# Kernel tuning notes

Measured on AMD Instinct MI355X. Metric: run time of the kernel, lower is better.

## Reference

```python
import jax, jax.numpy as jnp
import numpy as np

N, C, OUT, S, NS = 8192, 256, 256, 8, 16  # points, in_planes, out_planes, share_planes, nsample
MID = OUT  # mid_planes = out_planes // 1
H = OUT // S  # linear_w bottleneck width
EPS = 1e-5


def _bn(x, g, b, m, v):
    # inference-mode BatchNorm1d over last (channel) dim
    return (x - m) * jax.lax.rsqrt(v + EPS) * g + b


def _knn_idx(p, k):
    # squared euclidean distances, (N,N); indices of k nearest (self included)
    sq = jnp.sum(p * p, axis=1)
    d = sq[:, None] + sq[None, :] - 2.0 * (p @ p.T)
    return jax.lax.top_k(-jax.lax.stop_gradient(d), k)[1]  # (N, k) int32


def setup_inputs() -> dict:
    key = jax.random.key(0)
    ks = jax.random.split(key, 24)
    g = lambda i, shape, s=0.05: jax.random.normal(ks[i], shape, jnp.float32) * s
    u = lambda i, shape: jax.random.uniform(ks[i], shape, dtype=jnp.float32)
    return {
        'p': u(0, (N, 3)),
        'x': g(1, (N, C), 1.0),
        'w_q': g(2, (C, MID)), 'b_q': jnp.zeros((MID,), jnp.float32),
        'w_k': g(3, (C, MID)), 'b_k': jnp.zeros((MID,), jnp.float32),
        'w_v': g(4, (C, OUT)), 'b_v': jnp.zeros((OUT,), jnp.float32),
        'p_w1': g(5, (3, 3), 0.5), 'p_b1': jnp.zeros((3,), jnp.float32),
        'p_bn_g': u(6, (3,)) + 0.5, 'p_bn_b': g(7, (3,), 0.1),
        'p_bn_m': g(8, (3,), 0.1), 'p_bn_v': u(9, (3,)) + 0.5,
        'p_w2': g(10, (3, OUT), 0.5), 'p_b2': jnp.zeros((OUT,), jnp.float32),
        'w_bn1_g': u(11, (MID,)) + 0.5, 'w_bn1_b': g(12, (MID,), 0.1),
        'w_bn1_m': g(13, (MID,), 0.1), 'w_bn1_v': u(14, (MID,)) + 0.5,
        'w_l1_w': g(15, (MID, H)), 'w_l1_b': jnp.zeros((H,), jnp.float32),
        'w_bn2_g': u(16, (H,)) + 0.5, 'w_bn2_b': g(17, (H,), 0.1),
        'w_bn2_m': g(18, (H,), 0.1), 'w_bn2_v': u(19, (H,)) + 0.5,
        'w_l2_w': g(20, (H, H)), 'w_l2_b': jnp.zeros((H,), jnp.float32),
    }


def reference(p, x, w_q, b_q, w_k, b_k, w_v, b_v,
              p_w1, p_b1, p_bn_g, p_bn_b, p_bn_m, p_bn_v, p_w2, p_b2,
              w_bn1_g, w_bn1_b, w_bn1_m, w_bn1_v, w_l1_w, w_l1_b,
              w_bn2_g, w_bn2_b, w_bn2_m, w_bn2_v, w_l2_w, w_l2_b):
    # PointTransformerLayer forward (single point cloud, o = [N])
    xq = x @ w_q + b_q            # (N, MID)
    xk = x @ w_k + b_k            # (N, MID)
    xv = x @ w_v + b_v            # (N, OUT)

    idx = _knn_idx(p, NS)         # (N, NS) KNN neighbor indices
    pr_xyz = p[idx] - p[:, None, :]   # (N, NS, 3) relative coords (with_xyz=True)
    xk_g = xk[idx]                # (N, NS, MID) gathered keys
    xv_g = xv[idx]                # (N, NS, OUT) gathered values

    # linear_p: Linear(3,3) -> BN -> ReLU -> Linear(3, OUT)
    pr = jax.nn.relu(_bn(pr_xyz @ p_w1 + p_b1, p_bn_g, p_bn_b, p_bn_m, p_bn_v))
    pr = pr @ p_w2 + p_b2         # (N, NS, OUT)

    # einops reduce 'n ns (i j)->n ns j' with j=MID is identity since MID==OUT
    r_qk = xk_g - xq[:, None, :] + pr   # (N, NS, MID)

    # linear_w: BN -> ReLU -> Linear(MID,H) -> BN -> ReLU -> Linear(H,H)
    w = jax.nn.relu(_bn(r_qk, w_bn1_g, w_bn1_b, w_bn1_m, w_bn1_v)) @ w_l1_w + w_l1_b
    w = jax.nn.relu(_bn(w, w_bn2_g, w_bn2_b, w_bn2_m, w_bn2_v)) @ w_l2_w + w_l2_b
    w = jax.nn.softmax(w, axis=1)       # softmax over neighbors (dim=1)

    v = (xv_g + pr).reshape(N, NS, S, H)      # 'n ns (s i) -> n ns s i'
    out = jnp.einsum('ntsi,nti->nsi', v, w)   # weighted aggregation over neighbors
    return out.reshape(N, OUT)
```

## Files before the change

### kernel.cpp

```cpp
#include <hip/hip_runtime.h>
#include <hip/hip_bf16.h>
#include <math.h>

#define N_PTS 8192
#define C_IN  256
#define OUT_C 256
#define NSAMP 16
#define H_W   32
#define EPSBN 1e-5f
#define GDIM  8
#define NCELL (GDIM * GDIM * GDIM)
#define CAPC  768
#define CAP_H 96
#define GEMM_BLKS 384

typedef short bf16x8 __attribute__((ext_vector_type(8)));
typedef float f32x4  __attribute__((ext_vector_type(4)));

__device__ __forceinline__ float dist2(const float4 a, const float4 b) {
  float dot = a.x * b.x + a.y * b.y + a.z * b.z;
  return a.w + b.w - 2.0f * dot;
}

__device__ __forceinline__ unsigned long long make_key(float d, int j) {
  unsigned int di = __float_as_uint(d);
  unsigned int ord = ((int)di >= 0) ? (di ^ 0x80000000u) : ~di;
  return ((unsigned long long)ord << 32) | (unsigned int)j;
}

__device__ __forceinline__ void chain_insert(unsigned long long (&ak)[16], unsigned long long key) {
  if (key < ak[0]) {
    #pragma unroll
    for (int s = 0; s < 15; ++s) {
      unsigned long long mn = ak[s] < key ? ak[s] : key;
      unsigned long long nx = ak[s + 1];
      ak[s] = nx > mn ? nx : mn;
    }
    ak[15] = ak[15] < key ? ak[15] : key;
  }
}

__device__ __forceinline__ float b2f(short s) {
  return __uint_as_float(((unsigned int)(unsigned short)s) << 16);
}
__device__ __forceinline__ short f2b(float v) {
  __hip_bfloat16 h = __float2bfloat16(v);
  short s;
  __builtin_memcpy(&s, &h, 2);
  return s;
}

__global__ __launch_bounds__(256) void prep_kernel(
    const float* __restrict__ p, const float* __restrict__ x,
    const float* __restrict__ wq, const float* __restrict__ wk, const float* __restrict__ wv,
    const float* __restrict__ bq, const float* __restrict__ bk, const float* __restrict__ bv,
    const float* __restrict__ l1w, const float* __restrict__ l2w,
    const float* __restrict__ bn1g, const float* __restrict__ bn1b,
    const float* __restrict__ bn1m, const float* __restrict__ bn1v,
    float4* __restrict__ p4, __hip_bfloat16* __restrict__ Bp, float* __restrict__ biasp,
    __hip_bfloat16* __restrict__ xb,
    __hip_bfloat16* __restrict__ l1wp, __hip_bfloat16* __restrict__ l2wp,
    float* __restrict__ sc1, float* __restrict__ of1,
    int* __restrict__ cursor, int* __restrict__ pt_cell) {
  int tid = blockIdx.x * blockDim.x + threadIdx.x;
  if (tid < 262144) {
    const float* xr = &x[(size_t)tid * 8];
    float4 xa = *(const float4*)xr;
    float4 xc = *(const float4*)(xr + 4);
    bf16x8 v;
    v[0] = f2b(xa.x); v[1] = f2b(xa.y); v[2] = f2b(xa.z); v[3] = f2b(xa.w);
    v[4] = f2b(xc.x); v[5] = f2b(xc.y); v[6] = f2b(xc.z); v[7] = f2b(xc.w);
    *(bf16x8*)&xb[(size_t)tid * 8] = v;
  }
  if (tid < 48 * 32 * 16 * 8) {
    int kj = tid & 7, n = (tid >> 3) & 15, kb = (tid >> 7) & 31, nt = tid >> 12;
    int k = kb * 8 + kj, col = nt * 16 + n;
    float v;
    if (col < 256)      v = wq[k * 256 + col];
    else if (col < 512) v = wk[k * 256 + (col - 256)];
    else                v = wv[k * 256 + (col - 512)];
    Bp[tid] = __float2bfloat16(v);
  }
  if (tid < 768) {
    biasp[tid] = tid < 256 ? bq[tid] : (tid < 512 ? bk[tid - 256] : bv[tid - 512]);
  }
  if (tid < 8192) {
    int kj = tid & 7, n = (tid >> 3) & 15, kb = (tid >> 7) & 31, nt = (tid >> 12) & 1;
    int k = kb * 8 + kj, col = nt * 16 + n;
    l1wp[tid] = __float2bfloat16(l1w[k * 32 + col]);
  }
  if (tid < 1024) {
    int kj = tid & 7, n = (tid >> 3) & 15, kb = (tid >> 7) & 3, nt = (tid >> 9) & 1;
// ... 48 lines not shown
  rank[pid] = pos;
}

__global__ __launch_bounds__(256) void knn_gemm(
    const float4* __restrict__ sp4, const int* __restrict__ sidx,
    const int* __restrict__ cell_start, int* __restrict__ nbr,
    const __hip_bfloat16* __restrict__ xb, const __hip_bfloat16* __restrict__ Bp,
    const float* __restrict__ biasp, __hip_bfloat16* __restrict__ xqkv) {
  if (blockIdx.x < GEMM_BLKS) {
    const int w = threadIdx.x >> 6;
    const int lane = threadIdx.x & 63;
    const int gw = blockIdx.x * 4 + w;
    const int m0 = (gw & 127) * 64;
    const int nt4 = (gw >> 7) * 4;
    const int n = lane & 15, q = lane >> 4;

    int o[4];
    #pragma unroll
    for (int mi = 0; mi < 4; ++mi) o[mi] = sidx[m0 + mi * 16 + n];

    f32x4 acc[4][4];
    #pragma unroll
    for (int mi = 0; mi < 4; ++mi)
      #pragma unroll
      for (int ni = 0; ni < 4; ++ni) acc[mi][ni] = (f32x4){0.f, 0.f, 0.f, 0.f};

    for (int k0 = 0; k0 < 256; k0 += 32) {
      bf16x8 af[4], bfr[4];
      #pragma unroll
      for (int mi = 0; mi < 4; ++mi)
        af[mi] = *(const bf16x8*)&xb[(size_t)o[mi] * 256 + k0 + q * 8];
      #pragma unroll
      for (int ni = 0; ni < 4; ++ni)
        bfr[ni] = *(const bf16x8*)&Bp[(size_t)(nt4 + ni) * 4096 + (k0 >> 3) * 128 + q * 128 + n * 8];
      #pragma unroll
      for (int mi = 0; mi < 4; ++mi)
        #pragma unroll
        for (int ni = 0; ni < 4; ++ni)
          acc[mi][ni] = __builtin_amdgcn_mfma_f32_16x16x32_bf16(af[mi], bfr[ni], acc[mi][ni], 0, 0, 0);
    }
    #pragma unroll
    for (int ni = 0; ni < 4; ++ni) {
      int col = (nt4 + ni) * 16 + n;
      float b = biasp[col];
      #pragma unroll
      for (int mi = 0; mi < 4; ++mi)
        #pragma unroll
        for (int r = 0; r < 4; ++r)
          xqkv[(size_t)(m0 + mi * 16 + q * 4 + r) * 768 + col] = __float2bfloat16(acc[mi][ni][r] + b);
    }
    return;
  }

  const int kbid = blockIdx.x - GEMM_BLKS;
  const int cell = kbid >> 1;
  const int sub  = kbid & 1;
  const int cs = cell_start[cell], ce = cell_start[cell + 1];
  if (cs + 8 * sub >= ce) return;

  __shared__ float4 cpos[CAPC];
  __shared__ int    cidx[CAPC];
  __shared__ unsigned long long hk_s[8][CAP_H];
  __shared__ unsigned long long okey_s[8][16];
  __shared__ float tv_s[8][64];
  __shared__ int cnt_s[8];
  __shared__ int cell_s0_s[27];
  __shared__ int len_s[27];
  __shared__ int pref_s[28];
  __shared__ int nc_s, total_s;

  const int tid = threadIdx.x;
  const int hcx = cell & 7, hcy = (cell >> 3) & 7, hcz = cell >> 6;

  const int ax0 = max(hcx - 1, 0), ax1 = min(hcx + 1, GDIM - 1);
  const int ay0 = max(hcy - 1, 0), ay1 = min(hcy + 1, GDIM - 1);
  const int az0 = max(hcz - 1, 0), az1 = min(hcz + 1, GDIM - 1);
  const int nx = ax1 - ax0 + 1, ny = ay1 - ay0 + 1, nz = az1 - az0 + 1;
  const int nbc = nx * ny * nz;

  if (tid < nbc) {
    int cx = ax0 + tid % nx;
    int cy = ay0 + (tid / nx) % ny;
    int cz = az0 + tid / (nx * ny);
    int cc = (cz * GDIM + cy) * GDIM + cx;
    int s0 = cell_start[cc];
    cell_s0_s[tid] = s0;
    len_s[tid] = cell_start[cc + 1] - s0;
  }
  __syncthreads();
  if (tid == 0) {
    int off = 0;
    for (int m = 0; m < nbc; ++m) { pref_s[m] = off; off += len_s[m]; }
    pref_s[nbc] = off;
    nc_s = nbc;
    total_s = off;
  }
  __syncthreads();
  const int nc = nc_s, total = total_s;

  {
    const int grp = tid >> 5, ln = tid & 31;
    for (int m = grp; m < nbc; m += 8) {
      int base = pref_s[m], src = cell_s0_s[m];
      int lim = min(len_s[m], CAPC - base);
      for (int i = ln; i < lim; i += 32) {
        cpos[base + i] = sp4[src + i];
        cidx[base + i] = sidx[src + i];
      }
    }
  }
  __syncthreads();

  const int ptl = tid >> 5, slice = tid & 31;

  for (int p0 = cs + 8 * sub; p0 < ce; p0 += 16) {
    const int np = min(8, ce - p0);
    const bool pok = ptl < np;
    const int ld = pok ? (p0 + ptl) : cs;
    const float4 pi = sp4[ld];
    const int orig = sidx[ld];

    if (tid < 8) cnt_s[tid] = 0;
    if (tid < 128) okey_s[tid >> 4][tid & 15] = ~0ULL;
    __syncthreads();

    float t0 = 3.0e38f, t1 = 3.0e38f;
    for (int idx = slice; idx < total; idx += 32) {
      float4 q;
      if (idx < CAPC) q = cpos[idx];
      else {
        int c = 0;
        while (c + 1 < nc && pref_s[c + 1] <= idx) ++c;
        q = sp4[cell_s0_s[c] + (idx - pref_s[c])];
      }
      float d = dist2(pi, q);
      if (d < t1) {
        if (d < t0) { t1 = t0; t0 = d; } else { t1 = d; }
      }
    }
    tv_s[ptl][slice * 2]     = t0;
    tv_s[ptl][slice * 2 + 1] = t1;
    __syncthreads();

    int r0 = 0, r1 = 0;
    #pragma unroll 8
    for (int j = 0; j < 64; ++j) {
      float wv = tv_s[ptl][j];
      r0 += (wv < t0) ? 1 : 0;
      r1 += (wv < t1) ? 1 : 0;
    }
    float cand = fmaxf(r0 <= 15 ? t0 : -3.0e38f, r1 <= 15 ? t1 : -3.0e38f);
    cand = fmaxf(cand, __shfl_xor(cand, 1, 64));
    cand = fmaxf(cand, __shfl_xor(cand, 2, 64));
    cand = fmaxf(cand, __shfl_xor(cand, 4, 64));
    cand = fmaxf(cand, __shfl_xor(cand, 8, 64));
    cand = fmaxf(cand, __shfl_xor(cand, 16, 64));
    const float d16 = cand;

    const float rg = sqrtf(fmaxf(d16, 0.f)) * 1.001f + 1e-4f;
    const int lx = (int)fminf(fmaxf(floorf((pi.x - rg) * GDIM), 0.f), (float)(GDIM - 1));
    const int ux = (int)fminf(fmaxf(floorf((pi.x + rg) * GDIM), 0.f), (float)(GDIM - 1));
    const int ly = (int)fminf(fmaxf(floorf((pi.y - rg) * GDIM), 0.f), (float)(GDIM - 1));
    const int uy = (int)fminf(fmaxf(floorf((pi.y + rg) * GDIM), 0.f), (float)(GDIM - 1));
    const int lz = (int)fminf(fmaxf(floorf((pi.z - rg) * GDIM), 0.f), (float)(GDIM - 1));
    const int uz = (int)fminf(fmaxf(floorf((pi.z + rg) * GDIM), 0.f), (float)(GDIM - 1));
    const bool trigger = (lx < ax0 || ux > ax1 || ly < ay0 || uy > ay1 || lz < az0 || uz > az1);

    if (pok) {
      for (int idx = slice; idx < total; idx += 32) {
        float4 q;
        int qi;
        if (idx < CAPC) { q = cpos[idx]; qi = cidx[idx]; }
        else {
          int c = 0;
          while (c + 1 < nc && pref_s[c + 1] <= idx) ++c;
          int g = cell_s0_s[c] + (idx - pref_s[c]);
          q = sp4[g]; qi = sidx[g];
        }
        float d = dist2(pi, q);
        if (d <= d16) {
          int pos = atomicAdd(&cnt_s[ptl], 1);
          if (pos < CAP_H) hk_s[ptl][pos] = make_key(d, qi);
        }
      }
      if (trigger) {
        for (int cz = lz; cz <= uz; ++cz)
          for (int cy = ly; cy <= uy; ++cy)
            for (int cx = lx; cx <= ux; ++cx) {
              if (cx >= ax0 && cx <= ax1 && cy >= ay0 && cy <= ay1 && cz >= az0 && cz <= az1)
                continue;
              int cc = (cz * GDIM + cy) * GDIM + cx;
              int s0 = cell_start[cc], e0 = cell_start[cc + 1];
              for (int k = s0 + slice; k < e0; k += 32) {
                float d = dist2(pi, sp4[k]);
                if (d <= d16) {
                  int pos = atomicAdd(&cnt_s[ptl], 1);
                  if (pos < CAP_H) hk_s[ptl][pos] = make_key(d, sidx[k]);
                }
              }
            }
      }
    }
    __syncthreads();

    const int cntr = cnt_s[ptl];
    const bool overflow = cntr > CAP_H;
    const int cnt = overflow ? 0 : cntr;

    if (pok) {
      for (int i = slice; i < cnt; i += 32) {
        unsigned long long key = hk_s[ptl][i];
        int rk = 0;
        for (int j = 0; j < cnt; ++j) rk += (hk_s[ptl][j] < key) ? 1 : 0;
        if (rk < 16) okey_s[ptl][rk] = key;
      }
    }
    __syncthreads();

    if (!overflow) {
      if (pok && slice < 16) {
        unsigned long long key = okey_s[ptl][15 - slice];
        nbr[orig * NSAMP + slice] = (int)(key & 0xFFFFFFFFu);
      }
    } else if (pok && slice == 0) {
      unsigned long long akm[16];
      #pragma unroll
      for (int s = 0; s < 16; ++s) akm[s] = ~0ULL;
      for (int idx2 = 0; idx2 < total; ++idx2) {
        float4 q; int qi;
        if (idx2 < CAPC) { q = cpos[idx2]; qi = cidx[idx2]; }
        else {
          int c = 0;
          while (c + 1 < nc && pref_s[c + 1] <= idx2) ++c;
          int g = cell_s0_s[c] + (idx2 - pref_s[c]);
          q = sp4[g]; qi = sidx[g];
        }
        chain_insert(akm, make_key(dist2(pi, q), qi));
      }
      float r;
      if (akm[0] == ~0ULL) r = 1e9f;
      else {
        unsigned int ord = (unsigned int)(akm[0] >> 32);
        unsigned int di = (ord & 0x80000000u) ? (ord ^ 0x80000000u) : ~ord;
        float dd = __uint_as_float(di);
        r = sqrtf(fmaxf(dd, 0.f)) * 1.001f + 1e-4f;
      }
      int flx = (int)fminf(fmaxf(floorf((pi.x - r) * GDIM), 0.f), (float)(GDIM - 1));
      int fux = (int)fminf(fmaxf(floorf((pi.x + r) * GDIM), 0.f), (float)(GDIM - 1));
      int fly = (int)fminf(fmaxf(floorf((pi.y - r) * GDIM), 0.f), (float)(GDIM - 1));
      int fuy = (int)fminf(fmaxf(floorf((pi.y + r) * GDIM), 0.f), (float)(GDIM - 1));
      int flz = (int)fminf(fmaxf(floorf((pi.z - r) * GDIM), 0.f), (float)(GDIM - 1));
      int fuz = (int)fminf(fmaxf(floorf((pi.z + r) * GDIM), 0.f), (float)(GDIM - 1));
      for (int cz = flz; cz <= fuz; ++cz)
        for (int cy = fly; cy <= fuy; ++cy)
          for (int cx = flx; cx <= fux; ++cx) {
            if (cx >= ax0 && cx <= ax1 && cy >= ay0 && cy <= ay1 && cz >= az0 && cz <= az1)
              continue;
            int cc = (cz * GDIM + cy) * GDIM + cx;
            int s0 = cell_start[cc], e0 = cell_start[cc + 1];
            for (int k = s0; k < e0; ++k) {
              float4 q = sp4[k];
              chain_insert(akm, make_key(dist2(pi, q), sidx[k]));
            }
          }
      #pragma unroll
      for (int s = 0; s < 16; ++s) nbr[orig * NSAMP + s] = (int)(akm[s] & 0xFFFFFFFFu);
    }
    __syncthreads();
  }
}

__global__ __launch_bounds__(256) void fused_pt(
    const float4* __restrict__ sp4, const int* __restrict__ sidx, const int* __restrict__ rank,
    const __hip_bfloat16* __restrict__ xqkv, const int* __restrict__ nbr,
    const float* __restrict__ pw1, const float* __restrict__ pb1,
    const float* __restrict__ pbng, const float* __restrict__ pbnb,
    const float* __restrict__ pbnm, const float* __restrict__ pbnv,
    const float* __restrict__ pw2, const float* __restrict__ pb2,
    const float* __restrict__ sc1, const float* __restrict__ of1,
    const __hip_bfloat16* __restrict__ l1wp, const float* __restrict__ l1b,
    const float* __restrict__ bn2g, const float* __restrict__ bn2b,
    const float* __restrict__ bn2m, const float* __restrict__ bn2v,
    const __hip_bfloat16* __restrict__ l2wp, const float* __restrict__ l2b,
    float* __restrict__ out) {
  __shared__ __align__(16) __hip_bfloat16 a_s[2][NSAMP][264];
  __shared__ __align__(16) __hip_bfloat16 h1_s[2][NSAMP][40];
  __shared__ float w_s[2][NSAMP][33];
  __shared__ float q3_s[2][NSAMP][4];
  __shared__ int jn[2][NSAMP];
  __shared__ float psum[2][2][264];
  __shared__ int iorig[2];

  const int b0 = blockIdx.x * 2;
  const int tid = threadIdx.x;

  if (tid < 32) {
    int spt = tid >> 4, t = tid & 15;
    int b = b0 + spt;
    int i = sidx[b];
    if (t == 0) iorig[spt] = i;
    int j = nbr[i * NSAMP + t];
    int k = rank[j];
    jn[spt][t] = k;
    float4 pj = sp4[k];
    float4 pc = sp4[b];
    float rx = pj.x - pc.x;
    float ry = pj.y - pc.y;
    float rz = pj.z - pc.z;
    #pragma unroll
    for (int c3 = 0; c3 < 3; ++c3) {
      float t2 = rx * pw1[0 * 3 + c3] + ry * pw1[1 * 3 + c3] + rz * pw1[2 * 3 + c3] + pb1[c3];
      t2 = (t2 - pbnm[c3]) * rsqrtf(pbnv[c3] + EPSBN) * pbng[c3] + pbnb[c3];
      q3_s[spt][t][c3] = fmaxf(t2, 0.f);
    }
  }
  __syncthreads();

  const int pt = tid >> 7;
  const int t127 = tid & 127;
  const int g = t127 >> 5;
  const int cg = (t127 & 31) * 8;
  const int b = b0 + pt;

  float xqv[8], s1v[8], o1v[8], w20v[8], w21v[8], w22v[8], pb2v[8];
  {
    bf16x8 xq8 = *(const bf16x8*)&xqkv[(size_t)b * 768 + cg];
    #pragma unroll
    for (int u = 0; u < 8; ++u) {
      int c = cg + u;
      xqv[u] = b2f(xq8[u]);
      s1v[u] = sc1[c];
      o1v[u] = of1[c];
      w20v[u] = pw2[c];
      w21v[u] = pw2[256 + c];
      w22v[u] = pw2[512 + c];
      pb2v[u] = pb2[c];
    }
  }

  #pragma unroll
  for (int pass = 0; pass < 4; ++pass) {
    int t = g + pass * 4;
    int k = jn[pt][t];
    float q30 = q3_s[pt][t][0], q31 = q3_s[pt][t][1], q32 = q3_s[pt][t][2];
    bf16x8 xk8 = *(const bf16x8*)&xqkv[(size_t)k * 768 + 256 + cg];
    bf16x8 av;
    #pragma unroll
    for (int u = 0; u < 8; ++u) {
      float prv = q30 * w20v[u] + q31 * w21v[u] + q32 * w22v[u] + pb2v[u];
      float r = b2f(xk8[u]) - xqv[u] + prv;
      av[u] = f2b(fmaxf(r * s1v[u] + o1v[u], 0.f));
    }
    *(bf16x8*)&a_s[pt][t][cg] = av;
  }
  __syncthreads();

  const int w = tid >> 6;
  const int lane = tid & 63;
  const int mpt = w >> 1, hh = w & 1;
  const int nn = lane & 15, q = lane >> 4;
  {
    f32x4 acc = {0.f, 0.f, 0.f, 0.f};
    #pragma unroll
    for (int k0 = 0; k0 < 256; k0 += 32) {
      bf16x8 a = *(const bf16x8*)&a_s[mpt][nn][k0 + q * 8];
      bf16x8 bb = *(const bf16x8*)&l1wp[hh * 4096 + (k0 >> 3) * 128 + q * 128 + nn * 8];
      acc = __builtin_amdgcn_mfma_f32_16x16x32_bf16(a, bb, acc, 0, 0, 0);
    }
    int h = hh * 16 + nn;
    float s2 = bn2g[h] * rsqrtf(bn2v[h] + EPSBN);
    float o2 = bn2b[h] - bn2m[h] * s2;
    float l1bh = l1b[h];
    #pragma unroll
    for (int r = 0; r < 4; ++r)
      h1_s[mpt][q * 4 + r][h] = __float2bfloat16(fmaxf((acc[r] + l1bh) * s2 + o2, 0.f));
  }
  __syncthreads();

  {
    bf16x8 a = *(const bf16x8*)&h1_s[mpt][nn][q * 8];
    bf16x8 bb = *(const bf16x8*)&l2wp[hh * 512 + q * 128 + nn * 8];
    f32x4 z = {0.f, 0.f, 0.f, 0.f};
    f32x4 d = __builtin_amdgcn_mfma_f32_16x16x32_bf16(a, bb, z, 0, 0, 0);
    int h = hh * 16 + nn;
    float l2bh = l2b[h];
    #pragma unroll
    for (int r = 0; r < 4; ++r) w_s[mpt][q * 4 + r][h] = d[r] + l2bh;
  }
  __syncthreads();

  if (tid < 64) {
    int spt = tid >> 5, h = tid & 31;
    float m = -1e30f;
    #pragma unroll
    for (int t = 0; t < NSAMP; ++t) m = fmaxf(m, w_s[spt][t][h]);
    float e[NSAMP];
    float ssum = 0.f;
    #pragma unroll
    for (int t = 0; t < NSAMP; ++t) { e[t] = __expf(w_s[spt][t][h] - m); ssum += e[t]; }
    float inv = 1.f / ssum;
    #pragma unroll
    for (int t = 0; t < NSAMP; ++t) w_s[spt][t][h] = e[t] * inv;
  }
  __syncthreads();

  const int hb = cg & 31;
  float acc8[8];
  #pragma unroll
  for (int u = 0; u < 8; ++u) acc8[u] = 0.f;
  #pragma unroll
  for (int pass = 0; pass < 4; ++pass) {
    int t = g + pass * 4;
    int k = jn[pt][t];
    float q30 = q3_s[pt][t][0], q31 = q3_s[pt][t][1], q32 = q3_s[pt][t][2];
    bf16x8 xv8 = *(const bf16x8*)&xqkv[(size_t)k * 768 + 512 + cg];
    #pragma unroll
    for (int u = 0; u < 8; ++u) {
      float prv = q30 * w20v[u] + q31 * w21v[u] + q32 * w22v[u] + pb2v[u];
      acc8[u] += (b2f(xv8[u]) + prv) * w_s[pt][t][hb + u];
    }
  }
  #pragma unroll
  for (int u = 0; u < 8; ++u) acc8[u] += __shfl_xor(acc8[u], 32, 64);
  if ((lane >> 5) == 0) {
    #pragma unroll
    for (int u = 0; u < 8; ++u) psum[mpt][hh][cg + u] = acc8[u];
  }
  __syncthreads();
  {
    int opt = tid >> 7;
    int c0 = (tid & 127) * 2;
    float v0 = psum[opt][0][c0] + psum[opt][1][c0];
    float v1 = psum[opt][0][c0 + 1] + psum[opt][1][c0 + 1];
    int io = iorig[opt];
    *(float2*)&out[(size_t)io * OUT_C + c0] = make_float2(v0, v1);
  }
}

extern "C" void kernel_launch(void* const* d_in, const int* in_sizes, int n_in,
                              void* d_out, int out_size, void* d_ws, size_t ws_size,
                              hipStream_t stream) {
  const float* p    = (const float*)d_in[0];
  const float* x    = (const float*)d_in[1];
  const float* wq   = (const float*)d_in[2];
  const float* bq   = (const float*)d_in[3];
  const float* wk   = (const float*)d_in[4];
  const float* bk   = (const float*)d_in[5];
  const float* wv   = (const float*)d_in[6];
  const float* bv   = (const float*)d_in[7];
  const float* pw1  = (const float*)d_in[8];
  const float* pb1  = (const float*)d_in[9];
  const float* pbng = (const float*)d_in[10];
  const float* pbnb = (const float*)d_in[11];
  const float* pbnm = (const float*)d_in[12];
  const float* pbnv = (const float*)d_in[13];
  const float* pw2  = (const float*)d_in[14];
  const float* pb2  = (const float*)d_in[15];
  const float* bn1g = (const float*)d_in[16];
  const float* bn1b = (const float*)d_in[17];
  const float* bn1m = (const float*)d_in[18];
  const float* bn1v = (const float*)d_in[19];
  const float* l1w  = (const float*)d_in[20];
  const float* l1b  = (const float*)d_in[21];
  const float* bn2g = (const float*)d_in[22];
  const float* bn2b = (const float*)d_in[23];
  const float* bn2m = (const float*)d_in[24];
  const float* bn2v = (const float*)d_in[25];
  const float* l2w  = (const float*)d_in[26];
  const float* l2b  = (const float*)d_in[27];
  float* out = (float*)d_out;

  char* ws = (char*)d_ws;
  float4* p4       = (float4*)(ws + 0x000000);
  float*  biasp    = (float*)(ws + 0x040000);
  int*    cursor   = (int*)(ws + 0x042800);
  int*    cell_st  = (int*)(ws + 0x043000);
  int*    pt_cell  = (int*)(ws + 0x044000);
  float4* sp4      = (float4*)(ws + 0x050000);
  int*    sidx     = (int*)(ws + 0x070000);
  __hip_bfloat16* l1wp = (__hip_bfloat16*)(ws + 0x080000);
  __hip_bfloat16* l2wp = (__hip_bfloat16*)(ws + 0x084000);
  float*  sc1      = (float*)(ws + 0x085000);
  float*  of1      = (float*)(ws + 0x085800);
  int*    rank     = (int*)(ws + 0x088000);
  int*    nbr      = (int*)(ws + 0x090000);
  __hip_bfloat16* Bp   = (__hip_bfloat16*)(ws + 0x110000);
  __hip_bfloat16* xb   = (__hip_bfloat16*)(ws + 0x170000);
  __hip_bfloat16* xqkv = (__hip_bfloat16*)(ws + 0x570000);

  prep_kernel<<<dim3(1024), dim3(256), 0, stream>>>(
      p, x, wq, wk, wv, bq, bk, bv, l1w, l2w, bn1g, bn1b, bn1m, bn1v,
      p4, Bp, biasp, xb, l1wp, l2wp, sc1, of1, cursor, pt_cell);
  scatter_scan<<<dim3(16), dim3(512), 0, stream>>>(
      p4, pt_cell, cell_st, cursor, sp4, sidx, rank);
  knn_gemm<<<dim3(GEMM_BLKS + NCELL * 2), dim3(256), 0, stream>>>(
      sp4, sidx, cell_st, nbr, xb, Bp, biasp, xqkv);
  fused_pt<<<dim3(N_PTS / 2), dim3(256), 0, stream>>>(
      sp4, sidx, rank, xqkv, nbr, pw1, pb1, pbng, pbnb, pbnm, pbnv, pw2, pb2,
      sc1, of1, l1wp, l1b, bn2g, bn2b, bn2m, bn2v, l2wp, l2b, out);
}
```

Before: 197.9 us.

## Assign one wavefront per query point in KNN and drop shared-memory cell staging

The KNN part of the combined kernel is restructured so that each 64-lane wavefront handles one query point, with 2048 blocks of 4 points instead of two blocks per grid cell. Points are read directly from global memory over contiguous x-runs of the neighbouring cells, and the block-wide staging into shared memory and the __syncthreads barriers are removed. Candidate collection uses ballot/popcount compaction in place of shared atomics, and the final top-16 ranking is done with cross-lane shuffles. This removes per-cell load imbalance and barrier cost, but trades shared-memory reuse for repeated global/L2 reads and lowers the overflow buffer cap to 64.

```diff
diff --git a/kernel.cpp b/kernel.cpp
--- a/kernel.cpp
+++ b/kernel.cpp
@@ -10,9 +10,9 @@
 #define EPSBN 1e-5f
 #define GDIM  8
 #define NCELL (GDIM * GDIM * GDIM)
-#define CAPC  768
-#define CAP_H 96
+#define CAP_W 64
 #define GEMM_BLKS 384
+#define KNN_BLKS (N_PTS / 4)
 
 typedef short bf16x8 __attribute__((ext_vector_type(8)));
 typedef float f32x4  __attribute__((ext_vector_type(4)));
@@ -38,6 +38,18 @@
     }
     ak[15] = ak[15] < key ? ak[15] : key;
   }
+}
+
+__device__ __forceinline__ void ins2(float d, float& t0, float& t1) {
+  if (d < t1) {
+    if (d < t0) { t1 = t0; t0 = d; } else { t1 = d; }
+  }
+}
+
+__device__ __forceinline__ unsigned long long shfl64(unsigned long long v, int src) {
+  int lo = __shfl((int)(unsigned int)(v & 0xFFFFFFFFu), src, 64);
+  int hi = __shfl((int)(unsigned int)(v >> 32), src, 64);
+  return ((unsigned long long)(unsigned int)hi << 32) | (unsigned int)lo;
 }
 
 __device__ __forceinline__ float b2f(short s) {
@@ -192,221 +204,157 @@
     return;
   }
 
-  const int kbid = blockIdx.x - GEMM_BLKS;
-  const int cell = kbid >> 1;
-  const int sub  = kbid & 1;
-  const int cs = cell_start[cell], ce = cell_start[cell + 1];
-  if (cs + 8 * sub >= ce) return;
-
-  __shared__ float4 cpos[CAPC];
-  __shared__ int    cidx[CAPC];
-  __shared__ unsigned long long hk_s[8][CAP_H];
-  __shared__ unsigned long long okey_s[8][16];
-  __shared__ float tv_s[8][64];
-  __shared__ int cnt_s[8];
-  __shared__ int cell_s0_s[27];
-  __shared__ int len_s[27];
-  __shared__ int pref_s[28];
-  __shared__ int nc_s, total_s;
-
-  const int tid = threadIdx.x;
-  const int hcx = cell & 7, hcy = (cell >> 3) & 7, hcz = cell >> 6;
-
+  __shared__ unsigned long long buf_s[4][CAP_W];
+
+  const int wv = threadIdx.x >> 6;
+  const int lane = threadIdx.x & 63;
+  const int pid = (blockIdx.x - GEMM_BLKS) * 4 + wv;
+
+  const float4 pi = sp4[pid];
+  const int orig = sidx[pid];
+
+  const int hcx = min(GDIM - 1, max(0, (int)(pi.x * GDIM)));
+  const int hcy = min(GDIM - 1, max(0, (int)(pi.y * GDIM)));
+  const int hcz = min(GDIM - 1, max(0, (int)(pi.z * GDIM)));
   const int ax0 = max(hcx - 1, 0), ax1 = min(hcx + 1, GDIM - 1);
   const int ay0 = max(hcy - 1, 0), ay1 = min(hcy + 1, GDIM - 1);
   const int az0 = max(hcz - 1, 0), az1 = min(hcz + 1, GDIM - 1);
-  const int nx = ax1 - ax0 + 1, ny = ay1 - ay0 + 1, nz = az1 - az0 + 1;
-  const int nbc = nx * ny * nz;
-
-  if (tid < nbc) {
-    int cx = ax0 + tid % nx;
-    int cy = ay0 + (tid / nx) % ny;
-    int cz = az0 + tid / (nx * ny);
-    int cc = (cz * GDIM + cy) * GDIM + cx;
-    int s0 = cell_start[cc];
-    cell_s0_s[tid] = s0;
-    len_s[tid] = cell_start[cc + 1] - s0;
-  }
-  __syncthreads();
-  if (tid == 0) {
-    int off = 0;
-    for (int m = 0; m < nbc; ++m) { pref_s[m] = off; off += len_s[m]; }
-    pref_s[nbc] = off;
-    nc_s = nbc;
-    total_s = off;
-  }
-  __syncthreads();
-  const int nc = nc_s, total = total_s;
-
-  {
-    const int grp = tid >> 5, ln = tid & 31;
-    for (int m = grp; m < nbc; m += 8) {
-      int base = pref_s[m], src = cell_s0_s[m];
-      int lim = min(len_s[m], CAPC - base);
-      for (int i = ln; i < lim; i += 32) {
-        cpos[base + i] = sp4[src + i];
-        cidx[base + i] = sidx[src + i];
+
+  float t0 = 3.0e38f, t1 = 3.0e38f;
+  for (int cz = az0; cz <= az1; ++cz)
+    for (int cy = ay0; cy <= ay1; ++cy) {
+      int base = (cz * GDIM + cy) * GDIM;
+      int s = cell_start[base + ax0];
+      int e = cell_start[base + ax1 + 1];
+      for (int k = s + lane; k < e; k += 64) {
+        float d = dist2(pi, sp4[k]);
+        ins2(d, t0, t1);
       }
     }
-  }
-  __syncthreads();
-
-  const int ptl = tid >> 5, slice = tid & 31;
-
-  for (int p0 = cs + 8 * sub; p0 < ce; p0 += 16) {
-    const int np = min(8, ce - p0);
-    const bool pok = ptl < np;
-    const int ld = pok ? (p0 + ptl) : cs;
-    const float4 pi = sp4[ld];
-    const int orig = sidx[ld];
-
-    if (tid < 8) cnt_s[tid] = 0;
-    if (tid < 128) okey_s[tid >> 4][tid & 15] = ~0ULL;
-    __syncthreads();
-
-    float t0 = 3.0e38f, t1 = 3.0e38f;
-    for (int idx = slice; idx < total; idx += 32) {
-      float4 q;
-      if (idx < CAPC) q = cpos[idx];
-      else {
-        int c = 0;
-        while (c + 1 < nc && pref_s[c + 1] <= idx) ++c;
-        q = sp4[cell_s0_s[c] + (idx - pref_s[c])];
+
+  int r0 = 0, r1 = (t0 < t1) ? 1 : 0;
+  #pragma unroll 7
+  for (int s = 1; s < 64; ++s) {
+    float o0 = __shfl(t0, (lane + s) & 63, 64);
+    float o1 = __shfl(t1, (lane + s) & 63, 64);
+    r0 += (o0 < t0) ? 1 : 0;
+    r0 += (o1 < t0) ? 1 : 0;
+    r1 += (o0 < t1) ? 1 : 0;
+    r1 += (o1 < t1) ? 1 : 0;
+  }
+  float cand = fmaxf(r0 <= 15 ? t0 : -3.0e38f, r1 <= 15 ? t1 : -3.0e38f);
+  cand = fmaxf(cand, __shfl_xor(cand, 1, 64));
+  cand = fmaxf(cand, __shfl_xor(cand, 2, 64));
+  cand = fmaxf(cand, __shfl_xor(cand, 4, 64));
+  cand = fmaxf(cand, __shfl_xor(cand, 8, 64));
+  cand = fmaxf(cand, __shfl_xor(cand, 16, 64));
+  cand = fmaxf(cand, __shfl_xor(cand, 32, 64));
+  const float d16 = cand;
+
+  const float rg = sqrtf(fmaxf(d16, 0.f)) * 1.001f + 1e-4f;
+  const int lx = (int)fminf(fmaxf(floorf((pi.x - rg) * GDIM), 0.f), (float)(GDIM - 1));
+  const int ux = (int)fminf(fmaxf(floorf((pi.x + rg) * GDIM), 0.f), (float)(GDIM - 1));
+  const int ly = (int)fminf(fmaxf(floorf((pi.y - rg) * GDIM), 0.f), (float)(GDIM - 1));
+  const int uy = (int)fminf(fmaxf(floorf((pi.y + rg) * GDIM), 0.f), (float)(GDIM - 1));
+  const int lz = (int)fminf(fmaxf(floorf((pi.z - rg) * GDIM), 0.f), (float)(GDIM - 1));
+  const int uz = (int)fminf(fmaxf(floorf((pi.z + rg) * GDIM), 0.f), (float)(GDIM - 1));
+  const bool trigger = (lx < ax0 || ux > ax1 || ly < ay0 || uy > ay1 || lz < az0 || uz > az1);
+
+  const unsigned long long lmask = (1ULL << lane) - 1ULL;
+  int cnt = 0;
+  for (int cz = az0; cz <= az1; ++cz)
+    for (int cy = ay0; cy <= ay1; ++cy) {
+      int base = (cz * GDIM + cy) * GDIM;
+      int s = cell_start[base + ax0];
+      int e = cell_start[base + ax1 + 1];
+      int trips = (e - s + 63) >> 6;
+      for (int t = 0; t < trips; ++t) {
+        int idx = s + t * 64 + lane;
+        bool valid = idx < e;
+        int safei = valid ? idx : s;
+        float d = dist2(pi, sp4[safei]);
+        bool pred = valid && (d <= d16);
+        unsigned long long m = __ballot(pred);
+        if (pred) {
+          int pos = cnt + __popcll(m & lmask);
+          if (pos < CAP_W) buf_s[wv][pos] = make_key(d, sidx[idx]);
+        }
+        cnt += __popcll(m);
       }
-      float d = dist2(pi, q);
-      if (d < t1) {
-        if (d < t0) { t1 = t0; t0 = d; } else { t1 = d; }
+    }
+  if (trigger) {
+    for (int cz = lz; cz <= uz; ++cz)
+      for (int cy = ly; cy <= uy; ++cy)
+        for (int cx = lx; cx <= ux; ++cx) {
+          if (cx >= ax0 && cx <= ax1 && cy >= ay0 && cy <= ay1 && cz >= az0 && cz <= az1)
+            continue;
+          int cc = (cz * GDIM + cy) * GDIM + cx;
+          int s = cell_start[cc], e = cell_start[cc + 1];
+          int trips = (e - s + 63) >> 6;
+          for (int t = 0; t < trips; ++t) {
+            int idx = s + t * 64 + lane;
+            bool valid = idx < e;
+            int safei = valid ? idx : s;
+            float d = dist2(pi, sp4[safei]);
+            bool pred = valid && (d <= d16);
+            unsigned long long m = __ballot(pred);
+            if (pred) {
+              int pos = cnt + __popcll(m & lmask);
+              if (pos < CAP_W) buf_s[wv][pos] = make_key(d, sidx[idx]);
+            }
+            cnt += __popcll(m);
+          }
+        }
+  }
+
+  if (cnt <= CAP_W) {
+    unsigned long long key = (lane < cnt) ? buf_s[wv][lane] : ~0ULL;
+    int rk = 0;
+    #pragma unroll 7
+    for (int s = 1; s < 64; ++s) {
+      unsigned long long ko = shfl64(key, (lane + s) & 63);
+      rk += (ko < key) ? 1 : 0;
+    }
+    if (lane < cnt && rk < 16)
+      nbr[orig * NSAMP + (15 - rk)] = (int)(key & 0xFFFFFFFFu);
+  } else if (lane == 0) {
+    unsigned long long akm[16];
+    #pragma unroll
+    for (int s = 0; s < 16; ++s) akm[s] = ~0ULL;
+    for (int cz = az0; cz <= az1; ++cz)
+      for (int cy = ay0; cy <= ay1; ++cy) {
+        int base = (cz * GDIM + cy) * GDIM;
+        int s = cell_start[base + ax0];
+        int e = cell_start[base + ax1 + 1];
+        for (int k = s; k < e; ++k)
+          chain_insert(akm, make_key(dist2(pi, sp4[k]), sidx[k]));
       }
-    }
-    tv_s[ptl][slice * 2]     = t0;
-    tv_s[ptl][slice * 2 + 1] = t1;
-    __syncthreads();
-
-    int r0 = 0, r1 = 0;
-    #pragma unroll 8
-    for (int j = 0; j < 64; ++j) {
-      float wv = tv_s[ptl][j];
-      r0 += (wv < t0) ? 1 : 0;
-      r1 += (wv < t1) ? 1 : 0;
-    }
-    float cand = fmaxf(r0 <= 15 ? t0 : -3.0e38f, r1 <= 15 ? t1 : -3.0e38f);
-    cand = fmaxf(cand, __shfl_xor(cand, 1, 64));
-    cand = fmaxf(cand, __shfl_xor(cand, 2, 64));
-    cand = fmaxf(cand, __shfl_xor(cand, 4, 64));
-    cand = fmaxf(cand, __shfl_xor(cand, 8, 64));
-    cand = fmaxf(cand, __shfl_xor(cand, 16, 64));
-    const float d16 = cand;
-
-    const float rg = sqrtf(fmaxf(d16, 0.f)) * 1.001f + 1e-4f;
-    const int lx = (int)fminf(fmaxf(floorf((pi.x - rg) * GDIM), 0.f), (float)(GDIM - 1));
-    const int ux = (int)fminf(fmaxf(floorf((pi.x + rg) * GDIM), 0.f), (float)(GDIM - 1));
-    const int ly = (int)fminf(fmaxf(floorf((pi.y - rg) * GDIM), 0.f), (float)(GDIM - 1));
-    const int uy = (int)fminf(fmaxf(floorf((pi.y + rg) * GDIM), 0.f), (float)(GDIM - 1));
-    const int lz = (int)fminf(fmaxf(floorf((pi.z - rg) * GDIM), 0.f), (float)(GDIM - 1));
-    const int uz = (int)fminf(fmaxf(floorf((pi.z + rg) * GDIM), 0.f), (float)(GDIM - 1));
-    const bool trigger = (lx < ax0 || ux > ax1 || ly < ay0 || uy > ay1 || lz < az0 || uz > az1);
-
-    if (pok) {
-      for (int idx = slice; idx < total; idx += 32) {
-        float4 q;
-        int qi;
-        if (idx < CAPC) { q = cpos[idx]; qi = cidx[idx]; }
-        else {
-          int c = 0;
-          while (c + 1 < nc && pref_s[c + 1] <= idx) ++c;
-          int g = cell_s0_s[c] + (idx - pref_s[c]);
-          q = sp4[g]; qi = sidx[g];
+    float r;
+    if (akm[0] == ~0ULL) r = 1e9f;
+    else {
+      unsigned int ord = (unsigned int)(akm[0] >> 32);
+      unsigned int di = (ord & 0x80000000u) ? (ord ^ 0x80000000u) : ~ord;
+      float dd = __uint_as_float(di);
+      r = sqrtf(fmaxf(dd, 0.f)) * 1.001f + 1e-4f;
+    }
+    int flx = (int)fminf(fmaxf(floorf((pi.x - r) * GDIM), 0.f), (float)(GDIM - 1));
+    int fux = (int)fminf(fmaxf(floorf((pi.x + r) * GDIM), 0.f), (float)(GDIM - 1));
+    int fly = (int)fminf(fmaxf(floorf((pi.y - r) * GDIM), 0.f), (float)(GDIM - 1));
+    int fuy = (int)fminf(fmaxf(floorf((pi.y + r) * GDIM), 0.f), (float)(GDIM - 1));
+    int flz = (int)fminf(fmaxf(floorf((pi.z - r) * GDIM), 0.f), (float)(GDIM - 1));
+    int fuz = (int)fminf(fmaxf(floorf((pi.z + r) * GDIM), 0.f), (float)(GDIM - 1));
+    for (int cz = flz; cz <= fuz; ++cz)
+      for (int cy = fly; cy <= fuy; ++cy)
+        for (int cx = flx; cx <= fux; ++cx) {
+          if (cx >= ax0 && cx <= ax1 && cy >= ay0 && cy <= ay1 && cz >= az0 && cz <= az1)
+            continue;
+          int cc = (cz * GDIM + cy) * GDIM + cx;
+          int s0 = cell_start[cc], e0 = cell_start[cc + 1];
+          for (int k = s0; k < e0; ++k)
+            chain_insert(akm, make_key(dist2(pi, sp4[k]), sidx[k]));
         }
-        float d = dist2(pi, q);
-        if (d <= d16) {
-          int pos = atomicAdd(&cnt_s[ptl], 1);
-          if (pos < CAP_H) hk_s[ptl][pos] = make_key(d, qi);
-        }
-      }
-      if (trigger) {
-        for (int cz = lz; cz <= uz; ++cz)
-          for (int cy = ly; cy <= uy; ++cy)
-            for (int cx = lx; cx <= ux; ++cx) {
-              if (cx >= ax0 && cx <= ax1 && cy >= ay0 && cy <= ay1 && cz >= az0 && cz <= az1)
-                continue;
-              int cc = (cz * GDIM + cy) * GDIM + cx;
-              int s0 = cell_start[cc], e0 = cell_start[cc + 1];
-              for (int k = s0 + slice; k < e0; k += 32) {
-                float d = dist2(pi, sp4[k]);
-                if (d <= d16) {
-                  int pos = atomicAdd(&cnt_s[ptl], 1);
-                  if (pos < CAP_H) hk_s[ptl][pos] = make_key(d, sidx[k]);
-                }
-              }
-            }
-      }
-    }
-    __syncthreads();
-
-    const int cntr = cnt_s[ptl];
-    const bool overflow = cntr > CAP_H;
-    const int cnt = overflow ? 0 : cntr;
-
-    if (pok) {
-      for (int i = slice; i < cnt; i += 32) {
-        unsigned long long key = hk_s[ptl][i];
-        int rk = 0;
-        for (int j = 0; j < cnt; ++j) rk += (hk_s[ptl][j] < key) ? 1 : 0;
-        if (rk < 16) okey_s[ptl][rk] = key;
-      }
-    }
-    __syncthreads();
-
-    if (!overflow) {
-      if (pok && slice < 16) {
-        unsigned long long key = okey_s[ptl][15 - slice];
-        nbr[orig * NSAMP + slice] = (int)(key & 0xFFFFFFFFu);
-      }
-    } else if (pok && slice == 0) {
-      unsigned long long akm[16];
-      #pragma unroll
-      for (int s = 0; s < 16; ++s) akm[s] = ~0ULL;
-      for (int idx2 = 0; idx2 < total; ++idx2) {
-        float4 q; int qi;
-        if (idx2 < CAPC) { q = cpos[idx2]; qi = cidx[idx2]; }
-        else {
-          int c = 0;
-          while (c + 1 < nc && pref_s[c + 1] <= idx2) ++c;
-          int g = cell_s0_s[c] + (idx2 - pref_s[c]);
-          q = sp4[g]; qi = sidx[g];
-        }
-        chain_insert(akm, make_key(dist2(pi, q), qi));
-      }
-      float r;
-      if (akm[0] == ~0ULL) r = 1e9f;
-      else {
-        unsigned int ord = (unsigned int)(akm[0] >> 32);
-        unsigned int di = (ord & 0x80000000u) ? (ord ^ 0x80000000u) : ~ord;
-        float dd = __uint_as_float(di);
-        r = sqrtf(fmaxf(dd, 0.f)) * 1.001f + 1e-4f;
-      }
-      int flx = (int)fminf(fmaxf(floorf((pi.x - r) * GDIM), 0.f), (float)(GDIM - 1));
-      int fux = (int)fminf(fmaxf(floorf((pi.x + r) * GDIM), 0.f), (float)(GDIM - 1));
-      int fly = (int)fminf(fmaxf(floorf((pi.y - r) * GDIM), 0.f), (float)(GDIM - 1));
-      int fuy = (int)fminf(fmaxf(floorf((pi.y + r) * GDIM), 0.f), (float)(GDIM - 1));
-      int flz = (int)fminf(fmaxf(floorf((pi.z - r) * GDIM), 0.f), (float)(GDIM - 1));
-      int fuz = (int)fminf(fmaxf(floorf((pi.z + r) * GDIM), 0.f), (float)(GDIM - 1));
-      for (int cz = flz; cz <= fuz; ++cz)
-        for (int cy = fly; cy <= fuy; ++cy)
-          for (int cx = flx; cx <= fux; ++cx) {
-            if (cx >= ax0 && cx <= ax1 && cy >= ay0 && cy <= ay1 && cz >= az0 && cz <= az1)
-              continue;
-            int cc = (cz * GDIM + cy) * GDIM + cx;
-            int s0 = cell_start[cc], e0 = cell_start[cc + 1];
-            for (int k = s0; k < e0; ++k) {
-              float4 q = sp4[k];
-              chain_insert(akm, make_key(dist2(pi, q), sidx[k]));
-            }
-          }
-      #pragma unroll
-      for (int s = 0; s < 16; ++s) nbr[orig * NSAMP + s] = (int)(akm[s] & 0xFFFFFFFFu);
-    }
-    __syncthreads();
+    #pragma unroll
+    for (int s = 0; s < 16; ++s) nbr[orig * NSAMP + s] = (int)(akm[s] & 0xFFFFFFFFu);
   }
 }
 
@@ -633,7 +581,7 @@
       p4, Bp, biasp, xb, l1wp, l2wp, sc1, of1, cursor, pt_cell);
   scatter_scan<<<dim3(16), dim3(512), 0, stream>>>(
       p4, pt_cell, cell_st, cursor, sp4, sidx, rank);
-  knn_gemm<<<dim3(GEMM_BLKS + NCELL * 2), dim3(256), 0, stream>>>(
+  knn_gemm<<<dim3(GEMM_BLKS + KNN_BLKS), dim3(256), 0, stream>>>(
       sp4, sidx, cell_st, nbr, xb, Bp, biasp, xqkv);
   fused_pt<<<dim3(N_PTS / 2), dim3(256), 0, stream>>>(
       sp4, sidx, rank, xqkv, nbr, pw1, pb1, pbng, pbnb, pbnm, pbnv, pw2, pb2,
```

Measured after the change: 210.3 us. 6.3% more time.

## Make fused_pt wave-per-point, replacing block barriers with wave-local LDS waits

Applied to the files above, without the earlier changes.

The fused attention kernel now assigns one 64-lane wave to each point (four points per block) instead of two points per block split across waves. Because each wave owns its own shared-memory slices, the __syncthreads barriers become wave-local lgkmcnt waits, and the cross-wave partial-sum reduction through LDS is removed. Each wave now does both H halves of the MFMA GEMMs and all 16 neighbors of the final aggregation, so per-thread work and register use go up. The KNN inner loop change is cosmetic.

```diff
diff --git a/kernel.cpp b/kernel.cpp
--- a/kernel.cpp
+++ b/kernel.cpp
@@ -15,7 +15,14 @@
 #define GEMM_BLKS 384
 
 typedef short bf16x8 __attribute__((ext_vector_type(8)));
+typedef short bf16x4 __attribute__((ext_vector_type(4)));
 typedef float f32x4  __attribute__((ext_vector_type(4)));
+
+#define WSYNC() do { \
+  __builtin_amdgcn_sched_barrier(0); \
+  asm volatile("s_waitcnt lgkmcnt(0)" ::: "memory"); \
+  __builtin_amdgcn_sched_barrier(0); \
+} while (0)
 
 __device__ __forceinline__ float dist2(const float4 a, const float4 b) {
   float dot = a.x * b.x + a.y * b.y + a.z * b.z;
@@ -398,10 +405,8 @@
               continue;
             int cc = (cz * GDIM + cy) * GDIM + cx;
             int s0 = cell_start[cc], e0 = cell_start[cc + 1];
-            for (int k = s0; k < e0; ++k) {
-              float4 q = sp4[k];
-              chain_insert(akm, make_key(dist2(pi, q), sidx[k]));
-            }
+            for (int k = s0; k < e0; ++k)
+              chain_insert(akm, make_key(dist2(pi, sp4[k]), sidx[k]));
           }
       #pragma unroll
       for (int s = 0; s < 16; ++s) nbr[orig * NSAMP + s] = (int)(akm[s] & 0xFFFFFFFFu);
@@ -423,25 +428,22 @@
     const float* __restrict__ bn2m, const float* __restrict__ bn2v,
     const __hip_bfloat16* __restrict__ l2wp, const float* __restrict__ l2b,
     float* __restrict__ out) {
-  __shared__ __align__(16) __hip_bfloat16 a_s[2][NSAMP][264];
-  __shared__ __align__(16) __hip_bfloat16 h1_s[2][NSAMP][40];
-  __shared__ float w_s[2][NSAMP][33];
-  __shared__ float q3_s[2][NSAMP][4];
-  __shared__ int jn[2][NSAMP];
-  __shared__ float psum[2][2][264];
-  __shared__ int iorig[2];
-
-  const int b0 = blockIdx.x * 2;
-  const int tid = threadIdx.x;
-
-  if (tid < 32) {
-    int spt = tid >> 4, t = tid & 15;
-    int b = b0 + spt;
-    int i = sidx[b];
-    if (t == 0) iorig[spt] = i;
-    int j = nbr[i * NSAMP + t];
+  __shared__ __align__(16) __hip_bfloat16 a_s[4][NSAMP][264];
+  __shared__ __align__(16) __hip_bfloat16 h1_s[4][NSAMP][40];
+  __shared__ float w_s[4][NSAMP][33];
+  __shared__ float q3_s[4][NSAMP][4];
+  __shared__ int jn_s[4][NSAMP];
+
+  const int wv = threadIdx.x >> 6;
+  const int lane = threadIdx.x & 63;
+  const int b = blockIdx.x * 4 + wv;
+  const int io = sidx[b];
+
+  if (lane < 16) {
+    int t = lane;
+    int j = nbr[io * NSAMP + t];
     int k = rank[j];
-    jn[spt][t] = k;
+    jn_s[wv][t] = k;
     float4 pj = sp4[k];
     float4 pc = sp4[b];
     float rx = pj.x - pc.x;
@@ -451,129 +453,161 @@
     for (int c3 = 0; c3 < 3; ++c3) {
       float t2 = rx * pw1[0 * 3 + c3] + ry * pw1[1 * 3 + c3] + rz * pw1[2 * 3 + c3] + pb1[c3];
       t2 = (t2 - pbnm[c3]) * rsqrtf(pbnv[c3] + EPSBN) * pbng[c3] + pbnb[c3];
-      q3_s[spt][t][c3] = fmaxf(t2, 0.f);
-    }
-  }
-  __syncthreads();
-
-  const int pt = tid >> 7;
-  const int t127 = tid & 127;
-  const int g = t127 >> 5;
-  const int cg = (t127 & 31) * 8;
-  const int b = b0 + pt;
-
-  float xqv[8], s1v[8], o1v[8], w20v[8], w21v[8], w22v[8], pb2v[8];
+      q3_s[wv][t][c3] = fmaxf(t2, 0.f);
+    }
+  }
+  WSYNC();
+
   {
-    bf16x8 xq8 = *(const bf16x8*)&xqkv[(size_t)b * 768 + cg];
-    #pragma unroll
-    for (int u = 0; u < 8; ++u) {
-      int c = cg + u;
-      xqv[u] = b2f(xq8[u]);
-      s1v[u] = sc1[c];
-      o1v[u] = of1[c];
-      w20v[u] = pw2[c];
-      w21v[u] = pw2[256 + c];
-      w22v[u] = pw2[512 + c];
-      pb2v[u] = pb2[c];
-    }
-  }
-
-  #pragma unroll
-  for (int pass = 0; pass < 4; ++pass) {
-    int t = g + pass * 4;
-    int k = jn[pt][t];
-    float q30 = q3_s[pt][t][0], q31 = q3_s[pt][t][1], q32 = q3_s[pt][t][2];
-    bf16x8 xk8 = *(const bf16x8*)&xqkv[(size_t)k * 768 + 256 + cg];
-    bf16x8 av;
-    #pragma unroll
-    for (int u = 0; u < 8; ++u) {
-      float prv = q30 * w20v[u] + q31 * w21v[u] + q32 * w22v[u] + pb2v[u];
-      float r = b2f(xk8[u]) - xqv[u] + prv;
-      av[u] = f2b(fmaxf(r * s1v[u] + o1v[u], 0.f));
-    }
-    *(bf16x8*)&a_s[pt][t][cg] = av;
-  }
-  __syncthreads();
-
-  const int w = tid >> 6;
-  const int lane = tid & 63;
-  const int mpt = w >> 1, hh = w & 1;
+    const int c0 = (lane & 15) * 16;
+    bf16x8 xq0 = *(const bf16x8*)&xqkv[(size_t)b * 768 + c0];
+    bf16x8 xq1 = *(const bf16x8*)&xqkv[(size_t)b * 768 + c0 + 8];
+    float xqv[16], s1v[16], o1v[16], w20v[16], w21v[16], w22v[16], pb2v[16];
+    #pragma unroll
+    for (int u = 0; u < 8; ++u) { xqv[u] = b2f(xq0[u]); xqv[8 + u] = b2f(xq1[u]); }
+    #pragma unroll
+    for (int u4 = 0; u4 < 4; ++u4) {
+      float4 a0 = *(const float4*)&sc1[c0 + u4 * 4];
+      float4 a1 = *(const float4*)&of1[c0 + u4 * 4];
+      float4 a2 = *(const float4*)&pw2[c0 + u4 * 4];
+      float4 a3 = *(const float4*)&pw2[256 + c0 + u4 * 4];
+      float4 a4 = *(const float4*)&pw2[512 + c0 + u4 * 4];
+      float4 a5 = *(const float4*)&pb2[c0 + u4 * 4];
+      s1v[u4*4+0]=a0.x; s1v[u4*4+1]=a0.y; s1v[u4*4+2]=a0.z; s1v[u4*4+3]=a0.w;
+      o1v[u4*4+0]=a1.x; o1v[u4*4+1]=a1.y; o1v[u4*4+2]=a1.z; o1v[u4*4+3]=a1.w;
+      w20v[u4*4+0]=a2.x; w20v[u4*4+1]=a2.y; w20v[u4*4+2]=a2.z; w20v[u4*4+3]=a2.w;
+      w21v[u4*4+0]=a3.x; w21v[u4*4+1]=a3.y; w21v[u4*4+2]=a3.z; w21v[u4*4+3]=a3.w;
+      w22v[u4*4+0]=a4.x; w22v[u4*4+1]=a4.y; w22v[u4*4+2]=a4.z; w22v[u4*4+3]=a4.w;
+      pb2v[u4*4+0]=a5.x; pb2v[u4*4+1]=a5.y; pb2v[u4*4+2]=a5.z; pb2v[u4*4+3]=a5.w;
+    }
+    #pragma unroll
+    for (int pass = 0; pass < 4; ++pass) {
+      int t = (lane >> 4) + pass * 4;
+      int k = jn_s[wv][t];
+      float q30 = q3_s[wv][t][0], q31 = q3_s[wv][t][1], q32 = q3_s[wv][t][2];
+      bf16x8 xk0 = *(const bf16x8*)&xqkv[(size_t)k * 768 + 256 + c0];
+      bf16x8 xk1 = *(const bf16x8*)&xqkv[(size_t)k * 768 + 256 + c0 + 8];
+      bf16x8 av0, av1;
+      #pragma unroll
+      for (int u = 0; u < 8; ++u) {
+        float prv = q30 * w20v[u] + q31 * w21v[u] + q32 * w22v[u] + pb2v[u];
+        float r = b2f(xk0[u]) - xqv[u] + prv;
+        av0[u] = f2b(fmaxf(r * s1v[u] + o1v[u], 0.f));
+      }
+      #pragma unroll
+      for (int u = 0; u < 8; ++u) {
+        float prv = q30 * w20v[8+u] + q31 * w21v[8+u] + q32 * w22v[8+u] + pb2v[8+u];
+        float r = b2f(xk1[u]) - xqv[8+u] + prv;
+        av1[u] = f2b(fmaxf(r * s1v[8+u] + o1v[8+u], 0.f));
+      }
+      *(bf16x8*)&a_s[wv][t][c0] = av0;
+      *(bf16x8*)&a_s[wv][t][c0 + 8] = av1;
+    }
+  }
+  WSYNC();
+
   const int nn = lane & 15, q = lane >> 4;
+
   {
-    f32x4 acc = {0.f, 0.f, 0.f, 0.f};
+    f32x4 acc0 = {0.f, 0.f, 0.f, 0.f};
+    f32x4 acc1 = {0.f, 0.f, 0.f, 0.f};
     #pragma unroll
     for (int k0 = 0; k0 < 256; k0 += 32) {
-      bf16x8 a = *(const bf16x8*)&a_s[mpt][nn][k0 + q * 8];
-      bf16x8 bb = *(const bf16x8*)&l1wp[hh * 4096 + (k0 >> 3) * 128 + q * 128 + nn * 8];
-      acc = __builtin_amdgcn_mfma_f32_16x16x32_bf16(a, bb, acc, 0, 0, 0);
-    }
-    int h = hh * 16 + nn;
-    float s2 = bn2g[h] * rsqrtf(bn2v[h] + EPSBN);
-    float o2 = bn2b[h] - bn2m[h] * s2;
-    float l1bh = l1b[h];
-    #pragma unroll
-    for (int r = 0; r < 4; ++r)
-      h1_s[mpt][q * 4 + r][h] = __float2bfloat16(fmaxf((acc[r] + l1bh) * s2 + o2, 0.f));
-  }
-  __syncthreads();
+      bf16x8 a = *(const bf16x8*)&a_s[wv][nn][k0 + q * 8];
+      bf16x8 b0 = *(const bf16x8*)&l1wp[(k0 >> 3) * 128 + q * 128 + nn * 8];
+      bf16x8 b1 = *(const bf16x8*)&l1wp[4096 + (k0 >> 3) * 128 + q * 128 + nn * 8];
+      acc0 = __builtin_amdgcn_mfma_f32_16x16x32_bf16(a, b0, acc0, 0, 0, 0);
+      acc1 = __builtin_amdgcn_mfma_f32_16x16x32_bf16(a, b1, acc1, 0, 0, 0);
+    }
+    {
+      int h = nn;
+      float s2 = bn2g[h] * rsqrtf(bn2v[h] + EPSBN);
+      float o2 = bn2b[h] - bn2m[h] * s2;
+      float l1bh = l1b[h];
+      #pragma unroll
+      for (int r = 0; r < 4; ++r)
+        h1_s[wv][q * 4 + r][h] = __float2bfloat16(fmaxf((acc0[r] + l1bh) * s2 + o2, 0.f));
+    }
+    {
+      int h = 16 + nn;
+      float s2 = bn2g[h] * rsqrtf(bn2v[h] + EPSBN);
+      float o2 = bn2b[h] - bn2m[h] * s2;
+      float l1bh = l1b[h];
+      #pragma unroll
+      for (int r = 0; r < 4; ++r)
+        h1_s[wv][q * 4 + r][h] = __float2bfloat16(fmaxf((acc1[r] + l1bh) * s2 + o2, 0.f));
+    }
+  }
+  WSYNC();
 
   {
-    bf16x8 a = *(const bf16x8*)&h1_s[mpt][nn][q * 8];
-    bf16x8 bb = *(const bf16x8*)&l2wp[hh * 512 + q * 128 + nn * 8];
+    bf16x8 a2 = *(const bf16x8*)&h1_s[wv][nn][q * 8];
+    bf16x8 bb0 = *(const bf16x8*)&l2wp[q * 128 + nn * 8];
+    bf16x8 bb1 = *(const bf16x8*)&l2wp[512 + q * 128 + nn * 8];
     f32x4 z = {0.f, 0.f, 0.f, 0.f};
-    f32x4 d = __builtin_amdgcn_mfma_f32_16x16x32_bf16(a, bb, z, 0, 0, 0);
-    int h = hh * 16 + nn;
-    float l2bh = l2b[h];
-    #pragma unroll
-    for (int r = 0; r < 4; ++r) w_s[mpt][q * 4 + r][h] = d[r] + l2bh;
-  }
-  __syncthreads();
-
-  if (tid < 64) {
-    int spt = tid >> 5, h = tid & 31;
+    f32x4 d0 = __builtin_amdgcn_mfma_f32_16x16x32_bf16(a2, bb0, z, 0, 0, 0);
+    f32x4 d1 = __builtin_amdgcn_mfma_f32_16x16x32_bf16(a2, bb1, z, 0, 0, 0);
+    float l2b0 = l2b[nn], l2b1 = l2b[16 + nn];
+    #pragma unroll
+    for (int r = 0; r < 4; ++r) {
+      w_s[wv][q * 4 + r][nn] = d0[r] + l2b0;
+      w_s[wv][q * 4 + r][16 + nn] = d1[r] + l2b1;
+    }
+  }
+  WSYNC();
+
+  if (lane < 32) {
+    int h = lane;
     float m = -1e30f;
     #pragma unroll
-    for (int t = 0; t < NSAMP; ++t) m = fmaxf(m, w_s[spt][t][h]);
+    for (int t = 0; t < NSAMP; ++t) m = fmaxf(m, w_s[wv][t][h]);
     float e[NSAMP];
     float ssum = 0.f;
     #pragma unroll
-    for (int t = 0; t < NSAMP; ++t) { e[t] = __expf(w_s[spt][t][h] - m); ssum += e[t]; }
+    for (int t = 0; t < NSAMP; ++t) { e[t] = __expf(w_s[wv][t][h] - m); ssum += e[t]; }
     float inv = 1.f / ssum;
     #pragma unroll
-    for (int t = 0; t < NSAMP; ++t) w_s[spt][t][h] = e[t] * inv;
-  }
-  __syncthreads();
-
-  const int hb = cg & 31;
-  float acc8[8];
-  #pragma unroll
-  for (int u = 0; u < 8; ++u) acc8[u] = 0.f;
-  #pragma unroll
-  for (int pass = 0; pass < 4; ++pass) {
-    int t = g + pass * 4;
-    int k = jn[pt][t];
-    float q30 = q3_s[pt][t][0], q31 = q3_s[pt][t][1], q32 = q3_s[pt][t][2];
-    bf16x8 xv8 = *(const bf16x8*)&xqkv[(size_t)k * 768 + 512 + cg];
-    #pragma unroll
-    for (int u = 0; u < 8; ++u) {
-      float prv = q30 * w20v[u] + q31 * w21v[u] + q32 * w22v[u] + pb2v[u];
-      acc8[u] += (b2f(xv8[u]) + prv) * w_s[pt][t][hb + u];
-    }
-  }
-  #pragma unroll
-  for (int u = 0; u < 8; ++u) acc8[u] += __shfl_xor(acc8[u], 32, 64);
-  if ((lane >> 5) == 0) {
-    #pragma unroll
-    for (int u = 0; u < 8; ++u) psum[mpt][hh][cg + u] = acc8[u];
-  }
-  __syncthreads();
+    for (int t = 0; t < NSAMP; ++t) w_s[wv][t][h] = e[t] * inv;
+  }
+  WSYNC();
+
   {
-    int opt = tid >> 7;
-    int c0 = (tid & 127) * 2;
-    float v0 = psum[opt][0][c0] + psum[opt][1][c0];
-    float v1 = psum[opt][0][c0 + 1] + psum[opt][1][c0 + 1];
-    int io = iorig[opt];
-    *(float2*)&out[(size_t)io * OUT_C + c0] = make_float2(v0, v1);
+    const int pc0 = lane * 4;
+    const int hb = pc0 & 31;
+    float4 t20 = *(const float4*)&pw2[pc0];
+    float4 t21 = *(const float4*)&pw2[256 + pc0];
+    float4 t22 = *(const float4*)&pw2[512 + pc0];
+    float4 tb2 = *(const float4*)&pb2[pc0];
+    float w20p[4] = {t20.x, t20.y, t20.z, t20.w};
+    float w21p[4] = {t21.x, t21.y, t21.z, t21.w};
+    float w22p[4] = {t22.x, t22.y, t22.z, t22.w};
+    float pb2p[4] = {tb2.x, tb2.y, tb2.z, tb2.w};
+    float S[4][4];
+    #pragma unroll
+    for (int g = 0; g < 4; ++g)
+      #pragma unroll
+      for (int cc = 0; cc < 4; ++cc) S[g][cc] = 0.f;
+    #pragma unroll
+    for (int pass = 0; pass < 4; ++pass) {
+      #pragma unroll
+      for (int g = 0; g < 4; ++g) {
+        int t = g + pass * 4;
+        int k = jn_s[wv][t];
+        float q30 = q3_s[wv][t][0], q31 = q3_s[wv][t][1], q32 = q3_s[wv][t][2];
+        bf16x4 xv4 = *(const bf16x4*)&xqkv[(size_t)k * 768 + 512 + pc0];
+        #pragma unroll
+        for (int cc = 0; cc < 4; ++cc) {
+          float prv = q30 * w20p[cc] + q31 * w21p[cc] + q32 * w22p[cc] + pb2p[cc];
+          S[g][cc] += (b2f(xv4[cc]) + prv) * w_s[wv][t][hb + cc];
+        }
+      }
+    }
+    float4 res;
+    res.x = (S[0][0] + S[1][0]) + (S[2][0] + S[3][0]);
+    res.y = (S[0][1] + S[1][1]) + (S[2][1] + S[3][1]);
+    res.z = (S[0][2] + S[1][2]) + (S[2][2] + S[3][2]);
+    res.w = (S[0][3] + S[1][3]) + (S[2][3] + S[3][3]);
+    *(float4*)&out[(size_t)io * OUT_C + pc0] = res;
   }
 }
 
@@ -635,7 +669,7 @@
       p4, pt_cell, cell_st, cursor, sp4, sidx, rank);
   knn_gemm<<<dim3(GEMM_BLKS + NCELL * 2), dim3(256), 0, stream>>>(
       sp4, sidx, cell_st, nbr, xb, Bp, biasp, xqkv);
-  fused_pt<<<dim3(N_PTS / 2), dim3(256), 0, stream>>>(
+  fused_pt<<<dim3(N_PTS / 4), dim3(256), 0, stream>>>(
       sp4, sidx, rank, xqkv, nbr, pw1, pb1, pbng, pbnb, pbnm, pbnv, pw2, pb2,
       sc1, of1, l1wp, l1b, bn2g, bn2b, bn2m, bn2v, l2wp, l2b, out);
 }
```

Result: slower. 203.5 us (+2.8%).
